# Kernel tuning notes

Measured on AMD Instinct MI355X. Metric: run time of the kernel, lower is better.

Reference implementation:

```python
import jax, jax.numpy as jnp
import numpy as np

N_DIM = 16
E_DIM = 16
M_DIM = 16
HIDDEN = 64
N_EDGE = 1_600_000
N_NODE = 100_000


def setup_inputs() -> dict:
    key = jax.random.key(0)
    k1, k2, k3, k4, k5, k6, k7 = jax.random.split(key, 7)
    index_v = jax.random.randint(k1, (N_EDGE,), 0, N_NODE, dtype=jnp.int32)
    h_w = jax.random.normal(k2, (N_EDGE, N_DIM), dtype=jnp.float32)
    e_vw = jax.random.normal(k3, (N_EDGE, E_DIM), dtype=jnp.float32)
    # NNet params: Linear(e_dim, hidden) -> ReLU -> Linear(hidden, n_dim*m_dim)
    s1 = 1.0 / np.sqrt(E_DIM)
    s2 = 1.0 / np.sqrt(HIDDEN)
    W1 = jax.random.uniform(k4, (E_DIM, HIDDEN), jnp.float32, -s1, s1)
    b1 = jax.random.uniform(k5, (HIDDEN,), jnp.float32, -s1, s1)
    W2 = jax.random.uniform(k6, (HIDDEN, N_DIM * M_DIM), jnp.float32, -s2, s2)
    b2 = jax.random.uniform(k7, (N_DIM * M_DIM,), jnp.float32, -s2, s2)
    return {"index_v": index_v, "h_w": h_w, "e_vw": e_vw, "n_node": N_NODE,
            "W1": W1, "b1": b1, "W2": W2, "b2": b2}


def reference(index_v, h_w, e_vw, n_node, W1, b1, W2, b2):
    # Edge MLP: [n_edge, e_dim] -> [n_edge, n_dim*m_dim]
    hid = jax.nn.relu(e_vw @ W1 + b1)
    A_vw = (hid @ W2 + b2).reshape(-1, M_DIM, N_DIM)  # [n_edge, m_dim, n_dim]
    # Per-edge matvec: bmm(A_vw, h_w[:, :, None]) -> [n_edge, m_dim]
    m_vw = jnp.einsum("emn,en->em", A_vw, h_w)
    # Scatter-add messages to target nodes: [n_node, m_dim]
    m_v = jax.ops.segment_sum(m_vw, index_v, num_segments=n_node)
    return m_v
```

## Files before the change

### kernel.cpp

```cpp
#include <hip/hip_runtime.h>
#include <stdint.h>

typedef __bf16 bf16x8 __attribute__((ext_vector_type(8)));
typedef float  f32x4  __attribute__((ext_vector_type(4)));
typedef float  fvec4  __attribute__((ext_vector_type(4)));

#define EDIM   16
#define HIDDEN 64
#define MDIM   16
#define NDIM   16
#define KCHUNKS 32
#define NREP   8

__device__ __forceinline__ uint32_t pack_trunc(float x, float y) {
    return __builtin_amdgcn_perm(__builtin_bit_cast(uint32_t, x),
                                 __builtin_bit_cast(uint32_t, y),
                                 0x03020706u);
}

__device__ __forceinline__ uint16_t f32_to_bf16_rne(float f) {
    uint32_t u = __builtin_bit_cast(uint32_t, f);
    u += 0x7FFFu + ((u >> 16) & 1u);
    return (uint16_t)(u >> 16);
}

__device__ __forceinline__ bf16x8 u4_as_bf16x8(uint32_t a, uint32_t b,
                                               uint32_t c, uint32_t d) {
    union { uint32_t u[4]; bf16x8 v; } x;
    x.u[0] = a; x.u[1] = b; x.u[2] = c; x.u[3] = d;
    return x.v;
}

__device__ __forceinline__ void atomic_add_l2(float* p, float v) {
    asm volatile("global_atomic_add_f32 %0, %1, off"
                 :: "v"(p), "v"(v) : "memory");
}

template<int REPL>
__global__ __launch_bounds__(256, 4) void msg_mfma(
    const int*   __restrict__ idx,
    const float* __restrict__ h_w,
    const float* __restrict__ e_vw,
    const float* __restrict__ W1,
    const float* __restrict__ b1,
    const float* __restrict__ W2,
    const float* __restrict__ b2,
    float*       __restrict__ outb,
    int n_edge, int rep_stride)
{
    __align__(16) __shared__ ushort sB[KCHUNKS * 512];
    __align__(16) __shared__ ushort sHid[4 * 64 * 16];

    const int tid = threadIdx.x;

    float* out;
    if (REPL) {
        int xcd = __builtin_amdgcn_s_getreg(6164) & (NREP - 1);
        out = outb + (size_t)xcd * (size_t)rep_stride;
    } else {
        out = outb;
    }

    for (int t = tid; t < KCHUNKS * 512; t += 256) {
        int c = t >> 9, r = t & 511;
        int qq = r >> 7, m = (r >> 3) & 15, j = r & 7;
        int k = 2 * c + (qq >> 1);
        int n = ((qq & 1) << 3) + j;
        sB[t] = f32_to_bf16_rne(W2[k * 256 + m * 16 + n]);
    }

    const int lane = tid & 63;
    const int q    = lane >> 4;
    const int col  = lane & 15;
    const int w    = tid >> 6;

    uint32_t w1u[4][4];
    #pragma unroll
    for (int nt = 0; nt < 4; nt++) {
        #pragma unroll
        for (int d = 0; d < 4; d++) w1u[nt][d] = 0;
        #pragma unroll
        for (int j = 0; j < 8; j++) {
            int k = q * 8 + j;
            float v = 0.f;
            if (k < 16)       v = W1[k * 64 + nt * 16 + col];
            else if (k == 16) v = b1[nt * 16 + col];
            w1u[nt][j >> 1] |= ((uint32_t)f32_to_bf16_rne(v)) << ((j & 1) * 16);
        }
    }

    uint32_t b2u[4] = {0, 0, 0, 0};
    if (q < 2) {
        const float* bp = b2 + col * 16 + q * 8;
        #pragma unroll
        for (int j = 0; j < 8; j++)
            b2u[j >> 1] |= ((uint32_t)f32_to_bf16_rne(bp[j])) << ((j & 1) * 16);
    }
    __syncthreads();

    bf16x8 w1f[4];
    #pragma unroll
    for (int nt = 0; nt < 4; nt++)
        w1f[nt] = u4_as_bf16x8(w1u[nt][0], w1u[nt][1], w1u[nt][2], w1u[nt][3]);
    const bf16x8 b2f = u4_as_bf16x8(b2u[0], b2u[1], b2u[2], b2u[3]);

    const int nhalf = (q & 1) << 3;
    const int ntile = (n_edge + 15) >> 4;
    const int wave_id = blockIdx.x * 4 + w;
    const int wstride = gridDim.x * 4;
    if (wave_id >= ntile) return;

    const ushort* hidRd = &sHid[w * 1024 + (q >> 1) * 16 + col];
    ushort*       hidWr = &sHid[w * 1024 + col * 16 + q * 4];
    const ushort* bRd   = &sB[q * 128 + col * 8];

    int t = wave_id;
    fvec4 e0, e1, h0, h1; int4 nd;
    {
        int row = min(t * 16 + col, n_edge - 1);
        const fvec4* ep = (const fvec4*)(e_vw + (size_t)row * 16 + nhalf);
        e0 = __builtin_nontemporal_load(ep);
        e1 = __builtin_nontemporal_load(ep + 1);
        const fvec4* hp = (const fvec4*)(h_w + (size_t)row * 16 + nhalf);
        h0 = __builtin_nontemporal_load(hp);
        h1 = __builtin_nontemporal_load(hp + 1);
        int r0 = t * 16 + q * 4;
        nd.x = __builtin_nontemporal_load(idx + min(r0 + 0, n_edge - 1));
        nd.y = __builtin_nontemporal_load(idx + min(r0 + 1, n_edge - 1));
        nd.z = __builtin_nontemporal_load(idx + min(r0 + 2, n_edge - 1));
        nd.w = __builtin_nontemporal_load(idx + min(r0 + 3, n_edge - 1));
    }

    while (true) {
        int tn = t + wstride;
        bool have_next = (tn < ntile);
        fvec4 ne0, ne1, nh0, nh1; int4 nnd;
        if (have_next) {
            int row = min(tn * 16 + col, n_edge - 1);
            const fvec4* ep = (const fvec4*)(e_vw + (size_t)row * 16 + nhalf);
            ne0 = __builtin_nontemporal_load(ep);
            ne1 = __builtin_nontemporal_load(ep + 1);
            const fvec4* hp = (const fvec4*)(h_w + (size_t)row * 16 + nhalf);
            nh0 = __builtin_nontemporal_load(hp);
            nh1 = __builtin_nontemporal_load(hp + 1);
            int r0 = tn * 16 + q * 4;
            nnd.x = __builtin_nontemporal_load(idx + min(r0 + 0, n_edge - 1));
            nnd.y = __builtin_nontemporal_load(idx + min(r0 + 1, n_edge - 1));
            nnd.z = __builtin_nontemporal_load(idx + min(r0 + 2, n_edge - 1));
            nnd.w = __builtin_nontemporal_load(idx + min(r0 + 3, n_edge - 1));
        }

        uint32_t au0 = pack_trunc(e0.x, e0.y);
        uint32_t au1 = pack_trunc(e0.z, e0.w);
        uint32_t au2 = pack_trunc(e1.x, e1.y);
        uint32_t au3 = pack_trunc(e1.z, e1.w);
        if (q == 2) { au0 = 0x00003F80u; au1 = au2 = au3 = 0; }
        else if (q == 3) { au0 = au1 = au2 = au3 = 0; }
        bf16x8 av = u4_as_bf16x8(au0, au1, au2, au3);

        #pragma unroll
        for (int nt = 0; nt < 4; nt++) {
            f32x4 hc = {0.f, 0.f, 0.f, 0.f};
            hc = __builtin_amdgcn_mfma_f32_16x16x32_bf16(av, w1f[nt], hc, 0, 0, 0);
            uint32_t lo = pack_trunc(fmaxf(hc[0], 0.f), fmaxf(hc[1], 0.f));
            uint32_t hi = pack_trunc(fmaxf(hc[2], 0.f), fmaxf(hc[3], 0.f));
            *(uint2*)(hidWr + nt * 256) = make_uint2(lo, hi);
        }

        float hf[8] = {h0.x, h0.y, h0.z, h0.w, h1.x, h1.y, h1.z, h1.w};

        f32x4 acc = {0.f, 0.f, 0.f, 0.f};
        {
            uint32_t a0 = pack_trunc(hf[0], hf[1]);
            uint32_t a1 = pack_trunc(hf[2], hf[3]);
            uint32_t a2 = pack_trunc(hf[4], hf[5]);
            uint32_t a3 = pack_trunc(hf[6], hf[7]);
            bf16x8 af = u4_as_bf16x8(a0, a1, a2, a3);
            acc = __builtin_amdgcn_mfma_f32_16x16x32_bf16(af, b2f, acc, 0, 0, 0);
        }

        #pragma unroll
        for (int c = 0; c < KCHUNKS; c++) {
            uint16_t hk16 = hidRd[c * 32];
            float hk = __builtin_bit_cast(float, ((uint32_t)hk16) << 16);
            uint32_t a0 = pack_trunc(hk * hf[0], hk * hf[1]);
            uint32_t a1 = pack_trunc(hk * hf[2], hk * hf[3]);
            uint32_t a2 = pack_trunc(hk * hf[4], hk * hf[5]);
            uint32_t a3 = pack_trunc(hk * hf[6], hk * hf[7]);
            bf16x8 af = u4_as_bf16x8(a0, a1, a2, a3);
            bf16x8 bfb = *(const bf16x8*)(bRd + c * 512);
            acc = __builtin_amdgcn_mfma_f32_16x16x32_bf16(af, bfb, acc, 0, 0, 0);
        }

        int r0 = t * 16 + q * 4;
        if (REPL) {
            if (r0 + 0 < n_edge) atomic_add_l2(out + (size_t)nd.x * 16 + col, acc[0]);
            if (r0 + 1 < n_edge) atomic_add_l2(out + (size_t)nd.y * 16 + col, acc[1]);
            if (r0 + 2 < n_edge) atomic_add_l2(out + (size_t)nd.z * 16 + col, acc[2]);
            if (r0 + 3 < n_edge) atomic_add_l2(out + (size_t)nd.w * 16 + col, acc[3]);
        } else {
            if (r0 + 0 < n_edge) atomicAdd(out + (size_t)nd.x * 16 + col, acc[0]);
            if (r0 + 1 < n_edge) atomicAdd(out + (size_t)nd.y * 16 + col, acc[1]);
            if (r0 + 2 < n_edge) atomicAdd(out + (size_t)nd.z * 16 + col, acc[2]);
            if (r0 + 3 < n_edge) atomicAdd(out + (size_t)nd.w * 16 + col, acc[3]);
        }

        if (!have_next) break;
        t = tn;
        e0 = ne0; e1 = ne1; h0 = nh0; h1 = nh1; nd = nnd;
    }
}

__global__ void merge_rep(const fvec4* __restrict__ rep,
                          fvec4* __restrict__ out, int n4, int stride4)
{
    int i = blockIdx.x * blockDim.x + threadIdx.x;
    if (i >= n4) return;
    fvec4 s = rep[i];
    #pragma unroll
    for (int r = 1; r < NREP; r++)
        s += rep[(size_t)r * stride4 + i];
    out[i] = s;
}

extern "C" void kernel_launch(void* const* d_in, const int* in_sizes, int n_in,
                              void* d_out, int out_size, void* d_ws, size_t ws_size,
                              hipStream_t stream) {
    const int*   idx  = (const int*)  d_in[0];
    const float* h_w  = (const float*)d_in[1];
    const float* e_vw = (const float*)d_in[2];
    const float* W1   = (const float*)d_in[4];
    const float* b1   = (const float*)d_in[5];
    const float* W2   = (const float*)d_in[6];
    const float* b2   = (const float*)d_in[7];
    float* out = (float*)d_out;
    const int n_edge = in_sizes[0];

    const size_t out_floats = (size_t)out_size;
    const size_t need = (size_t)NREP * out_floats * sizeof(float);

    if (ws_size >= need && (out_floats & 3) == 0) {
        float* rep = (float*)d_ws;
        hipMemsetAsync(rep, 0, need, stream);
        msg_mfma<1><<<2048, 256, 0, stream>>>(idx, h_w, e_vw, W1, b1, W2, b2,
                                              rep, n_edge, (int)out_floats);
        const int n4 = (int)(out_floats >> 2);
        const int mblocks = (n4 + 255) / 256;
        merge_rep<<<mblocks, 256, 0, stream>>>((const fvec4*)rep, (fvec4*)out,
                                               n4, n4);
    } else {
        hipMemsetAsync(out, 0, out_floats * sizeof(float), stream);
        msg_mfma<0><<<2048, 256, 0, stream>>>(idx, h_w, e_vw, W1, b1, W2, b2,
                                              out, n_edge, 0);
    }
}
```

Baseline: 341.0 us.

## Use 512-thread blocks, packed multiplies, scalar-base atomics and full-tile fast path

Blocks grow from 4 to 8 waves, which halves the per-wave cost of staging W2 into shared memory, and the grid drops to 1536 blocks. The per-chunk scaling of h by the hidden activation now uses v_pk_mul_f32. The atomics take a scalar base plus a 32-bit offset, which cuts 64-bit address arithmetic. A full-tile fast path skips the bounds clamps and checks. The risks are higher register pressure under the new launch bounds and 32-bit offset overflow on very large outputs.

Result: faster. 324.6 us (-4.8%).

```diff
diff --git a/kernel.cpp b/kernel.cpp
--- a/kernel.cpp
+++ b/kernel.cpp
@@ -4,6 +4,7 @@
 typedef __bf16 bf16x8 __attribute__((ext_vector_type(8)));
 typedef float  f32x4  __attribute__((ext_vector_type(4)));
 typedef float  fvec4  __attribute__((ext_vector_type(4)));
+typedef float  f32x2  __attribute__((ext_vector_type(2)));
 
 #define EDIM   16
 #define HIDDEN 64
@@ -11,6 +12,7 @@
 #define NDIM   16
 #define KCHUNKS 32
 #define NREP   8
+#define WPB    8
 
 __device__ __forceinline__ uint32_t pack_trunc(float x, float y) {
     return __builtin_amdgcn_perm(__builtin_bit_cast(uint32_t, x),
@@ -31,13 +33,20 @@
     return x.v;
 }
 
-__device__ __forceinline__ void atomic_add_l2(float* p, float v) {
-    asm volatile("global_atomic_add_f32 %0, %1, off"
-                 :: "v"(p), "v"(v) : "memory");
+__device__ __forceinline__ f32x2 pk_mul(f32x2 a, f32x2 b) {
+    f32x2 d;
+    asm("v_pk_mul_f32 %0, %1, %2" : "=v"(d) : "v"(a), "v"(b));
+    return d;
+}
+
+__device__ __forceinline__ void atomic_add_s(const float* base, uint32_t off,
+                                             float v) {
+    asm volatile("global_atomic_add_f32 %0, %1, %2"
+                 :: "v"(off), "v"(v), "s"(base) : "memory");
 }
 
 template<int REPL>
-__global__ __launch_bounds__(256, 4) void msg_mfma(
+__global__ __launch_bounds__(512, 6) void msg_mfma(
     const int*   __restrict__ idx,
     const float* __restrict__ h_w,
     const float* __restrict__ e_vw,
@@ -49,11 +58,11 @@
     int n_edge, int rep_stride)
 {
     __align__(16) __shared__ ushort sB[KCHUNKS * 512];
-    __align__(16) __shared__ ushort sHid[4 * 64 * 16];
+    __align__(16) __shared__ ushort sHid[WPB * 64 * 16];
 
     const int tid = threadIdx.x;
 
-    float* out;
+    const float* out;
     if (REPL) {
         int xcd = __builtin_amdgcn_s_getreg(6164) & (NREP - 1);
         out = outb + (size_t)xcd * (size_t)rep_stride;
@@ -61,7 +70,7 @@
         out = outb;
     }
 
-    for (int t = tid; t < KCHUNKS * 512; t += 256) {
+    for (int t = tid; t < KCHUNKS * 512; t += 512) {
         int c = t >> 9, r = t & 511;
         int qq = r >> 7, m = (r >> 3) & 15, j = r & 7;
         int k = 2 * c + (qq >> 1);
@@ -106,48 +115,69 @@
 
     const int nhalf = (q & 1) << 3;
     const int ntile = (n_edge + 15) >> 4;
-    const int wave_id = blockIdx.x * 4 + w;
-    const int wstride = gridDim.x * 4;
+    const int wave_id = blockIdx.x * WPB + w;
+    const int wstride = gridDim.x * WPB;
     if (wave_id >= ntile) return;
 
     const ushort* hidRd = &sHid[w * 1024 + (q >> 1) * 16 + col];
     ushort*       hidWr = &sHid[w * 1024 + col * 16 + q * 4];
     const ushort* bRd   = &sB[q * 128 + col * 8];
+    const uint32_t col4 = (uint32_t)col * 4u;
 
     int t = wave_id;
-    fvec4 e0, e1, h0, h1; int4 nd;
+    fvec4 e0, e1, h0, h1; int4 nd; bool full;
     {
-        int row = min(t * 16 + col, n_edge - 1);
-        const fvec4* ep = (const fvec4*)(e_vw + (size_t)row * 16 + nhalf);
+        int rbase = t * 16;
+        full = (rbase + 16 <= n_edge);
+        int row = full ? (rbase + col) : min(rbase + col, n_edge - 1);
+        uint32_t ro = (uint32_t)row * 16u + (uint32_t)nhalf;
+        const fvec4* ep = (const fvec4*)(e_vw + ro);
         e0 = __builtin_nontemporal_load(ep);
         e1 = __builtin_nontemporal_load(ep + 1);
-        const fvec4* hp = (const fvec4*)(h_w + (size_t)row * 16 + nhalf);
+        const fvec4* hp = (const fvec4*)(h_w + ro);
         h0 = __builtin_nontemporal_load(hp);
         h1 = __builtin_nontemporal_load(hp + 1);
-        int r0 = t * 16 + q * 4;
-        nd.x = __builtin_nontemporal_load(idx + min(r0 + 0, n_edge - 1));
-        nd.y = __builtin_nontemporal_load(idx + min(r0 + 1, n_edge - 1));
-        nd.z = __builtin_nontemporal_load(idx + min(r0 + 2, n_edge - 1));
-        nd.w = __builtin_nontemporal_load(idx + min(r0 + 3, n_edge - 1));
+        int r0 = rbase + q * 4;
+        if (full) {
+            nd.x = __builtin_nontemporal_load(idx + r0 + 0);
+            nd.y = __builtin_nontemporal_load(idx + r0 + 1);
+            nd.z = __builtin_nontemporal_load(idx + r0 + 2);
+            nd.w = __builtin_nontemporal_load(idx + r0 + 3);
+        } else {
+            nd.x = __builtin_nontemporal_load(idx + min(r0 + 0, n_edge - 1));
+            nd.y = __builtin_nontemporal_load(idx + min(r0 + 1, n_edge - 1));
+            nd.z = __builtin_nontemporal_load(idx + min(r0 + 2, n_edge - 1));
+            nd.w = __builtin_nontemporal_load(idx + min(r0 + 3, n_edge - 1));
+        }
     }
 
     while (true) {
         int tn = t + wstride;
         bool have_next = (tn < ntile);
-        fvec4 ne0, ne1, nh0, nh1; int4 nnd;
+        fvec4 ne0, ne1, nh0, nh1; int4 nnd; bool nfull = false;
         if (have_next) {
-            int row = min(tn * 16 + col, n_edge - 1);
-            const fvec4* ep = (const fvec4*)(e_vw + (size_t)row * 16 + nhalf);
+            int rbase = tn * 16;
+            nfull = (rbase + 16 <= n_edge);
+            int row = nfull ? (rbase + col) : min(rbase + col, n_edge - 1);
+            uint32_t ro = (uint32_t)row * 16u + (uint32_t)nhalf;
+            const fvec4* ep = (const fvec4*)(e_vw + ro);
             ne0 = __builtin_nontemporal_load(ep);
             ne1 = __builtin_nontemporal_load(ep + 1);
-            const fvec4* hp = (const fvec4*)(h_w + (size_t)row * 16 + nhalf);
+            const fvec4* hp = (const fvec4*)(h_w + ro);
             nh0 = __builtin_nontemporal_load(hp);
             nh1 = __builtin_nontemporal_load(hp + 1);
-            int r0 = tn * 16 + q * 4;
-            nnd.x = __builtin_nontemporal_load(idx + min(r0 + 0, n_edge - 1));
-            nnd.y = __builtin_nontemporal_load(idx + min(r0 + 1, n_edge - 1));
-            nnd.z = __builtin_nontemporal_load(idx + min(r0 + 2, n_edge - 1));
-            nnd.w = __builtin_nontemporal_load(idx + min(r0 + 3, n_edge - 1));
+            int r0 = rbase + q * 4;
+            if (nfull) {
+                nnd.x = __builtin_nontemporal_load(idx + r0 + 0);
+                nnd.y = __builtin_nontemporal_load(idx + r0 + 1);
+                nnd.z = __builtin_nontemporal_load(idx + r0 + 2);
+                nnd.w = __builtin_nontemporal_load(idx + r0 + 3);
+            } else {
+                nnd.x = __builtin_nontemporal_load(idx + min(r0 + 0, n_edge - 1));
+                nnd.y = __builtin_nontemporal_load(idx + min(r0 + 1, n_edge - 1));
+                nnd.z = __builtin_nontemporal_load(idx + min(r0 + 2, n_edge - 1));
+                nnd.w = __builtin_nontemporal_load(idx + min(r0 + 3, n_edge - 1));
+            }
         }
 
         uint32_t au0 = pack_trunc(e0.x, e0.y);
@@ -167,47 +197,64 @@
             *(uint2*)(hidWr + nt * 256) = make_uint2(lo, hi);
         }
 
-        float hf[8] = {h0.x, h0.y, h0.z, h0.w, h1.x, h1.y, h1.z, h1.w};
+        f32x2 hp0; hp0.x = h0.x; hp0.y = h0.y;
+        f32x2 hp1; hp1.x = h0.z; hp1.y = h0.w;
+        f32x2 hp2; hp2.x = h1.x; hp2.y = h1.y;
+        f32x2 hp3; hp3.x = h1.z; hp3.y = h1.w;
 
         f32x4 acc = {0.f, 0.f, 0.f, 0.f};
         {
-            uint32_t a0 = pack_trunc(hf[0], hf[1]);
-            uint32_t a1 = pack_trunc(hf[2], hf[3]);
-            uint32_t a2 = pack_trunc(hf[4], hf[5]);
-            uint32_t a3 = pack_trunc(hf[6], hf[7]);
+            uint32_t a0 = pack_trunc(hp0.x, hp0.y);
+            uint32_t a1 = pack_trunc(hp1.x, hp1.y);
+            uint32_t a2 = pack_trunc(hp2.x, hp2.y);
+            uint32_t a3 = pack_trunc(hp3.x, hp3.y);
             bf16x8 af = u4_as_bf16x8(a0, a1, a2, a3);
             acc = __builtin_amdgcn_mfma_f32_16x16x32_bf16(af, b2f, acc, 0, 0, 0);
         }
 
         #pragma unroll
         for (int c = 0; c < KCHUNKS; c++) {
-            uint16_t hk16 = hidRd[c * 32];
-            float hk = __builtin_bit_cast(float, ((uint32_t)hk16) << 16);
-            uint32_t a0 = pack_trunc(hk * hf[0], hk * hf[1]);
-            uint32_t a1 = pack_trunc(hk * hf[2], hk * hf[3]);
-            uint32_t a2 = pack_trunc(hk * hf[4], hk * hf[5]);
-            uint32_t a3 = pack_trunc(hk * hf[6], hk * hf[7]);
+            uint32_t hku = ((uint32_t)hidRd[c * 32]) << 16;
+            float hkf = __builtin_bit_cast(float, hku);
+            f32x2 hk2; hk2.x = hkf; hk2.y = hkf;
+            f32x2 p0 = pk_mul(hk2, hp0);
+            f32x2 p1 = pk_mul(hk2, hp1);
+            f32x2 p2 = pk_mul(hk2, hp2);
+            f32x2 p3 = pk_mul(hk2, hp3);
+            uint32_t a0 = pack_trunc(p0.x, p0.y);
+            uint32_t a1 = pack_trunc(p1.x, p1.y);
+            uint32_t a2 = pack_trunc(p2.x, p2.y);
+            uint32_t a3 = pack_trunc(p3.x, p3.y);
             bf16x8 af = u4_as_bf16x8(a0, a1, a2, a3);
             bf16x8 bfb = *(const bf16x8*)(bRd + c * 512);
             acc = __builtin_amdgcn_mfma_f32_16x16x32_bf16(af, bfb, acc, 0, 0, 0);
         }
 
-        int r0 = t * 16 + q * 4;
         if (REPL) {
-            if (r0 + 0 < n_edge) atomic_add_l2(out + (size_t)nd.x * 16 + col, acc[0]);
-            if (r0 + 1 < n_edge) atomic_add_l2(out + (size_t)nd.y * 16 + col, acc[1]);
-            if (r0 + 2 < n_edge) atomic_add_l2(out + (size_t)nd.z * 16 + col, acc[2]);
-            if (r0 + 3 < n_edge) atomic_add_l2(out + (size_t)nd.w * 16 + col, acc[3]);
+            if (full) {
+                atomic_add_s(out, (uint32_t)nd.x * 64u + col4, acc[0]);
+                atomic_add_s(out, (uint32_t)nd.y * 64u + col4, acc[1]);
+                atomic_add_s(out, (uint32_t)nd.z * 64u + col4, acc[2]);
+                atomic_add_s(out, (uint32_t)nd.w * 64u + col4, acc[3]);
+            } else {
+                int r0 = t * 16 + q * 4;
+                if (r0 + 0 < n_edge) atomic_add_s(out, (uint32_t)nd.x * 64u + col4, acc[0]);
+                if (r0 + 1 < n_edge) atomic_add_s(out, (uint32_t)nd.y * 64u + col4, acc[1]);
+                if (r0 + 2 < n_edge) atomic_add_s(out, (uint32_t)nd.z * 64u + col4, acc[2]);
+                if (r0 + 3 < n_edge) atomic_add_s(out, (uint32_t)nd.w * 64u + col4, acc[3]);
+            }
         } else {
-            if (r0 + 0 < n_edge) atomicAdd(out + (size_t)nd.x * 16 + col, acc[0]);
-            if (r0 + 1 < n_edge) atomicAdd(out + (size_t)nd.y * 16 + col, acc[1]);
-            if (r0 + 2 < n_edge) atomicAdd(out + (size_t)nd.z * 16 + col, acc[2]);
-            if (r0 + 3 < n_edge) atomicAdd(out + (size_t)nd.w * 16 + col, acc[3]);
+            float* o = (float*)out;
+            int r0 = t * 16 + q * 4;
+            if (r0 + 0 < n_edge) atomicAdd(o + (size_t)nd.x * 16 + col, acc[0]);
+            if (r0 + 1 < n_edge) atomicAdd(o + (size_t)nd.y * 16 + col, acc[1]);
+            if (r0 + 2 < n_edge) atomicAdd(o + (size_t)nd.z * 16 + col, acc[2]);
+            if (r0 + 3 < n_edge) atomicAdd(o + (size_t)nd.w * 16 + col, acc[3]);
         }
 
         if (!have_next) break;
         t = tn;
-        e0 = ne0; e1 = ne1; h0 = nh0; h1 = nh1; nd = nnd;
+        e0 = ne0; e1 = ne1; h0 = nh0; h1 = nh1; nd = nnd; full = nfull;
     }
 }
 
@@ -242,7 +289,7 @@
     if (ws_size >= need && (out_floats & 3) == 0) {
         float* rep = (float*)d_ws;
         hipMemsetAsync(rep, 0, need, stream);
-        msg_mfma<1><<<2048, 256, 0, stream>>>(idx, h_w, e_vw, W1, b1, W2, b2,
+        msg_mfma<1><<<1536, 512, 0, stream>>>(idx, h_w, e_vw, W1, b1, W2, b2,
                                               rep, n_edge, (int)out_floats);
         const int n4 = (int)(out_floats >> 2);
         const int mblocks = (n4 + 255) / 256;
@@ -250,7 +297,7 @@
                                                n4, n4);
     } else {
         hipMemsetAsync(out, 0, out_floats * sizeof(float), stream);
-        msg_mfma<0><<<2048, 256, 0, stream>>>(idx, h_w, e_vw, W1, b1, W2, b2,
+        msg_mfma<0><<<1536, 512, 0, stream>>>(idx, h_w, e_vw, W1, b1, W2, b2,
                                               out, n_edge, 0);
     }
 }
```
